# Optimization experiments

Hardware: AMD Instinct MI355X
Metric: run time of the kernel (lower is better)

The kernel has to match this reference:

```python
import jax, jax.numpy as jnp
import numpy as np

N_NODES = 100000
N_EDGES = 400000
IN_F, HID, OUT_F = 128, 1024, 64


def gcn_conv(x, src, dst, ew, W, b, n):
    # PyG GCNConv: add self-loops (weight 1), symmetric normalization,
    # out[dst] += norm * (x @ W)[src], then bias.
    loop = jnp.arange(n)
    s = jnp.concatenate([src, loop])
    d = jnp.concatenate([dst, loop])
    w = jnp.concatenate([ew, jnp.ones((n,), dtype=ew.dtype)])
    deg = jax.ops.segment_sum(w, d, num_segments=n)
    dinv = jnp.where(deg > 0, jax.lax.rsqrt(deg), 0.0)
    norm = dinv[s] * w * dinv[d]                      # [E+N]
    h = x @ W                                         # [N, out]
    out = jax.ops.segment_sum(h[s] * norm[:, None], d, num_segments=n)
    return out + b


def setup_inputs() -> dict:
    key = jax.random.key(0)
    k = jax.random.split(key, 8)
    x = jax.random.normal(k[0], (N_NODES, IN_F), dtype=jnp.float32)
    edge_index = jax.random.randint(k[1], (2, N_EDGES), 0, N_NODES, dtype=jnp.int64)
    edge_weight = jax.random.uniform(k[2], (N_EDGES,), dtype=jnp.float32)
    # Glorot-ish init for params
    W1 = jax.random.normal(k[3], (IN_F, HID), dtype=jnp.float32) * (1.0 / np.sqrt(IN_F))
    b1 = jnp.zeros((HID,), dtype=jnp.float32)
    W2 = jax.random.normal(k[4], (HID, OUT_F), dtype=jnp.float32) * (1.0 / np.sqrt(HID))
    b2 = jnp.zeros((OUT_F,), dtype=jnp.float32)
    return {"x": x, "edge_index": edge_index, "edge_weight": edge_weight,
            "W1": W1, "b1": b1, "W2": W2, "b2": b2}


def reference(x, edge_index, edge_weight, W1, b1, W2, b2):
    src, dst = edge_index[0], edge_index[1]
    h = gcn_conv(x, src, dst, edge_weight, W1, b1, N_NODES)
    h = jax.nn.relu(h)
    # F.dropout with training=False is identity (eval mode)
    out = gcn_conv(h, src, dst, edge_weight, W2, b2, N_NODES)
    return out
```

## Files before the change

### kernel.cpp

```cpp
#include <hip/hip_runtime.h>
#include <hip/hip_bf16.h>

#define N_NODES 100000
#define N_EDGES 400000
#define IN_F    128
#define HID     1024
#define OUT_F   64
#define BUCKET_CAP 24

typedef __attribute__((ext_vector_type(8))) short short8;
typedef __attribute__((ext_vector_type(4))) float floatx4;

__device__ inline unsigned short f2bf(float f) {
    unsigned int u = __float_as_uint(f);
    unsigned int r = u + 0x7FFF + ((u >> 16) & 1);
    return (unsigned short)(r >> 16);
}

__device__ inline unsigned int cvtpk(float a, float b) {
    union { __hip_bfloat162 h; unsigned int u; } v;
    v.h = __float22bfloat162_rn(float2{a, b});
    return v.u;
}

__device__ inline float bf2f(unsigned int lo16) {
    return __uint_as_float(lo16 << 16);
}

__device__ __forceinline__ void gload_lds16(const void* g, void* l) {
    __builtin_amdgcn_global_load_lds(
        (const __attribute__((address_space(1))) void*)g,
        (__attribute__((address_space(3))) void*)l, 16, 0, 0);
}

#define XB_BLOCKS  6250
#define WSB_BLOCKS 768
#define DEG_BLOCKS 1563

__global__ __launch_bounds__(256) void setup_kernel(
    const float* __restrict__ x, unsigned short* __restrict__ xb,
    const float* __restrict__ W1, const float* __restrict__ W2,
    unsigned short* __restrict__ S,
    const int* __restrict__ dst, const float* __restrict__ ew,
    float* __restrict__ deg)
{
    int b = blockIdx.x;
    int tid = threadIdx.x;
    if (b < XB_BLOCKS) {
        long i = (long)b * 256 + tid;
        float4 a = ((const float4*)x)[i * 2];
        float4 c = ((const float4*)x)[i * 2 + 1];
        ((uint4*)xb)[i] = make_uint4(cvtpk(a.x, a.y), cvtpk(a.z, a.w),
                                     cvtpk(c.x, c.y), cvtpk(c.z, c.w));
    } else if (b < XB_BLOCKS + WSB_BLOCKS) {
        int idx = b - XB_BLOCKS;
        int c = idx / 48;
        int r = (idx % 48) * 256 + tid;
        int f = r >> 9;
        int l = (r >> 3) & 63;
        int j = r & 7;
        float v;
        if (f < 16) {
            int nt = f >> 2, kt = f & 3;
            int hid = c * 64 + nt * 16 + (l & 15);
            int k   = kt * 32 + (l >> 4) * 8 + j;
            v = W1[(long)k * HID + hid];
        } else {
            int f2 = f - 16;
            int kb = f2 >> 2, nt2 = f2 & 3;
            int kh = c * 64 + kb * 32 + (j >> 2) * 16 + (l >> 4) * 4 + (j & 3);
            int oc = nt2 * 16 + (l & 15);
            v = W2[(long)kh * OUT_F + oc];
        }
        S[(long)c * 12288 + r] = f2bf(v);
    } else {
        int e = (b - XB_BLOCKS - WSB_BLOCKS) * 256 + tid;
        if (e < N_EDGES) atomicAdd(&deg[dst[e]], ew[e]);
    }
}

__global__ void fill_pairs_kernel(const int* __restrict__ src, const int* __restrict__ dst,
                                  const float* __restrict__ w, const float* __restrict__ deg,
                                  int* __restrict__ cnt, int2* __restrict__ pairs, int E) {
    int e = blockIdx.x * blockDim.x + threadIdx.x;
    if (e < E) {
        int s = src[e];
        int d = dst[e];
        float nv = rsqrtf(deg[s] + 1.0f) * w[e] * rsqrtf(deg[d] + 1.0f);
        int slot = atomicAdd(&cnt[d], 1);
        if (slot < BUCKET_CAP)
            pairs[(long)d * BUCKET_CAP + slot] = make_int2(s, __float_as_int(nv));
    }
}


__global__ __launch_bounds__(256) void gather128_kernel(
    const int2* __restrict__ pairs, const int* __restrict__ cnt,
    const float* __restrict__ deg, const unsigned short* __restrict__ xb,
    unsigned short* __restrict__ xab)
{
    int node = blockIdx.x * 16 + (threadIdx.x >> 4);
    int l = threadIdx.x & 15;
    float di = rsqrtf(deg[node] + 1.0f);
    float s = di * di;
    uint4 uv = ((const uint4*)(xb + (long)node * IN_F))[l];
    float acc[8];
    acc[0] = bf2f(uv.x & 0xffffu) * s; acc[1] = bf2f(uv.x >> 16) * s;
    acc[2] = bf2f(uv.y & 0xffffu) * s; acc[3] = bf2f(uv.y >> 16) * s;
    acc[4] = bf2f(uv.z & 0xffffu) * s; acc[5] = bf2f(uv.z >> 16) * s;
    acc[6] = bf2f(uv.w & 0xffffu) * s; acc[7] = bf2f(uv.w >> 16) * s;
    int c = cnt[node]; c = c < BUCKET_CAP ? c : BUCKET_CAP;
    const int2* p = pairs + (long)node * BUCKET_CAP;
    int j = 0;
    for (; j + 4 <= c; j += 4) {
        int4 q01 = *(const int4*)(p + j);
        int4 q23 = *(const int4*)(p + j + 2);
        uint4 u0 = ((const uint4*)(xb + (long)q01.x * IN_F))[l];
        uint4 u1 = ((const uint4*)(xb + (long)q01.z * IN_F))[l];
        uint4 u2 = ((const uint4*)(xb + (long)q23.x * IN_F))[l];
        uint4 u3 = ((const uint4*)(xb + (long)q23.z * IN_F))[l];
        float n0 = __int_as_float(q01.y), n1 = __int_as_float(q01.w);
        float n2 = __int_as_float(q23.y), n3 = __int_as_float(q23.w);
        acc[0] += n0 * bf2f(u0.x & 0xffffu) + n1 * bf2f(u1.x & 0xffffu)
                + n2 * bf2f(u2.x & 0xffffu) + n3 * bf2f(u3.x & 0xffffu);
        acc[1] += n0 * bf2f(u0.x >> 16) + n1 * bf2f(u1.x >> 16)
                + n2 * bf2f(u2.x >> 16) + n3 * bf2f(u3.x >> 16);
        acc[2] += n0 * bf2f(u0.y & 0xffffu) + n1 * bf2f(u1.y & 0xffffu)
                + n2 * bf2f(u2.y & 0xffffu) + n3 * bf2f(u3.y & 0xffffu);
        acc[3] += n0 * bf2f(u0.y >> 16) + n1 * bf2f(u1.y >> 16)
                + n2 * bf2f(u2.y >> 16) + n3 * bf2f(u3.y >> 16);
        acc[4] += n0 * bf2f(u0.z & 0xffffu) + n1 * bf2f(u1.z & 0xffffu)
                + n2 * bf2f(u2.z & 0xffffu) + n3 * bf2f(u3.z & 0xffffu);
        acc[5] += n0 * bf2f(u0.z >> 16) + n1 * bf2f(u1.z >> 16)
                + n2 * bf2f(u2.z >> 16) + n3 * bf2f(u3.z >> 16);
        acc[6] += n0 * bf2f(u0.w & 0xffffu) + n1 * bf2f(u1.w & 0xffffu)
                + n2 * bf2f(u2.w & 0xffffu) + n3 * bf2f(u3.w & 0xffffu);
        acc[7] += n0 * bf2f(u0.w >> 16) + n1 * bf2f(u1.w >> 16)
                + n2 * bf2f(u2.w >> 16) + n3 * bf2f(u3.w >> 16);
    }
    for (; j < c; j++) {
        int2 pp = p[j];
        float nv = __int_as_float(pp.y);
        uint4 u = ((const uint4*)(xb + (long)pp.x * IN_F))[l];
        acc[0] += nv * bf2f(u.x & 0xffffu); acc[1] += nv * bf2f(u.x >> 16);
        acc[2] += nv * bf2f(u.y & 0xffffu); acc[3] += nv * bf2f(u.y >> 16);
        acc[4] += nv * bf2f(u.z & 0xffffu); acc[5] += nv * bf2f(u.z >> 16);
        acc[6] += nv * bf2f(u.w & 0xffffu); acc[7] += nv * bf2f(u.w >> 16);
    }
    uint4 pk = make_uint4(cvtpk(acc[0], acc[1]), cvtpk(acc[2], acc[3]),
                          cvtpk(acc[4], acc[5]), cvtpk(acc[6], acc[7]));
    ((uint4*)(xab + (long)node * IN_F))[l] = pk;
}

__global__ __launch_bounds__(256) void gather64_kernel(
    const int2* __restrict__ pairs, const int* __restrict__ cnt,
    const float* __restrict__ deg, const unsigned short* __restrict__ tb,
    const float* __restrict__ bias, float* __restrict__ out)
{
    int node = blockIdx.x * 16 + (threadIdx.x >> 4);
    int l = threadIdx.x & 15;
    float di = rsqrtf(deg[node] + 1.0f);
    float s = di * di;
    uint2 tv = ((const uint2*)(tb + (long)node * OUT_F))[l];
    float4 bb = ((const float4*)bias)[l];
    float4 acc;
    acc.x = bf2f(tv.x & 0xffffu) * s + bb.x;
    acc.y = bf2f(tv.x >> 16) * s + bb.y;
    acc.z = bf2f(tv.y & 0xffffu) * s + bb.z;
    acc.w = bf2f(tv.y >> 16) * s + bb.w;
    int c = cnt[node]; c = c < BUCKET_CAP ? c : BUCKET_CAP;
    const int2* p = pairs + (long)node * BUCKET_CAP;
    int j = 0;
    for (; j + 4 <= c; j += 4) {
        int4 q01 = *(const int4*)(p + j);
        int4 q23 = *(const int4*)(p + j + 2);
        uint2 u0 = ((const uint2*)(tb + (long)q01.x * OUT_F))[l];
        uint2 u1 = ((const uint2*)(tb + (long)q01.z * OUT_F))[l];
        uint2 u2 = ((const uint2*)(tb + (long)q23.x * OUT_F))[l];
        uint2 u3 = ((const uint2*)(tb + (long)q23.z * OUT_F))[l];
        float n0 = __int_as_float(q01.y), n1 = __int_as_float(q01.w);
        float n2 = __int_as_float(q23.y), n3 = __int_as_float(q23.w);
        acc.x += n0 * bf2f(u0.x & 0xffffu) + n1 * bf2f(u1.x & 0xffffu)
               + n2 * bf2f(u2.x & 0xffffu) + n3 * bf2f(u3.x & 0xffffu);
        acc.y += n0 * bf2f(u0.x >> 16) + n1 * bf2f(u1.x >> 16)
               + n2 * bf2f(u2.x >> 16) + n3 * bf2f(u3.x >> 16);
        acc.z += n0 * bf2f(u0.y & 0xffffu) + n1 * bf2f(u1.y & 0xffffu)
               + n2 * bf2f(u2.y & 0xffffu) + n3 * bf2f(u3.y & 0xffffu);
        acc.w += n0 * bf2f(u0.y >> 16) + n1 * bf2f(u1.y >> 16)
               + n2 * bf2f(u2.y >> 16) + n3 * bf2f(u3.y >> 16);
    }
    for (; j < c; j++) {
        int2 pp = p[j];
        float nv = __int_as_float(pp.y);
        uint2 u = ((const uint2*)(tb + (long)pp.x * OUT_F))[l];
        acc.x += nv * bf2f(u.x & 0xffffu);
        acc.y += nv * bf2f(u.x >> 16);
        acc.z += nv * bf2f(u.y & 0xffffu);
        acc.w += nv * bf2f(u.y >> 16);
    }
    ((float4*)(out + (long)node * OUT_F))[l] = acc;
}


__global__ __launch_bounds__(512, 4) void fused_mlp_mfma_kernel(
    const unsigned short* __restrict__ Xb, const unsigned short* __restrict__ Wstream,
    const float* __restrict__ b1, unsigned short* __restrict__ Tb, int M)
{
    __shared__ unsigned short Wbuf[2][12288];

    const int tid = threadIdx.x;
    const int w   = tid >> 6;
    const int l   = tid & 63;
    const int lr  = l & 15;
    const int lq  = l >> 4;
    const long row0 = (long)blockIdx.x * 256 + w * 32;

    short8 bx[2][4];
    #pragma unroll
    for (int rt = 0; rt < 2; rt++) {
        long row = row0 + rt * 16 + lr;
        if (row < M) {
            const unsigned short* p = Xb + row * IN_F + lq * 8;
            #pragma unroll
            for (int kt = 0; kt < 4; kt++)
                bx[rt][kt] = *(const short8*)(p + kt * 32);
        } else {
            #pragma unroll
            for (int kt = 0; kt < 4; kt++)
                #pragma unroll
                for (int j = 0; j < 8; j++) bx[rt][kt][j] = 0;
        }
    }

    {
        const unsigned short* g = Wstream + (long)(w * 3) * 512 + l * 8;
        unsigned short* d = &Wbuf[0][(w * 3) * 512];
        #pragma unroll
        for (int s = 0; s < 3; s++)
            gload_lds16(g + s * 512, d + s * 512);
    }
    __syncthreads();

    floatx4 tacc[2][4];
    #pragma unroll
    for (int rt = 0; rt < 2; rt++)
        #pragma unroll
        for (int nt = 0; nt < 4; nt++)
            tacc[rt][nt] = (floatx4)0.0f;

    for (int c = 0; c < 16; c++) {
        const unsigned short* Wb = &Wbuf[c & 1][0];

        if (c < 15) {
            const unsigned short* g = Wstream + (long)(c + 1) * 12288 + (long)(w * 3) * 512 + l * 8;
            unsigned short* d = &Wbuf[(c + 1) & 1][(w * 3) * 512];
            #pragma unroll
            for (int s = 0; s < 3; s++)
                gload_lds16(g + s * 512, d + s * 512);
        }

        #pragma unroll
        for (int h = 0; h < 2; h++) {
            floatx4 hacc[2][2];
            #pragma unroll
            for (int rt = 0; rt < 2; rt++)
                #pragma unroll
                for (int n = 0; n < 2; n++)
                    hacc[rt][n] = (floatx4)0.0f;

            #pragma unroll
            for (int n = 0; n < 2; n++) {
                const int nt = h * 2 + n;
                short8 w1f[4];
                #pragma unroll
                for (int kt = 0; kt < 4; kt++)
                    w1f[kt] = *(const short8*)(Wb + (nt * 4 + kt) * 512 + l * 8);
                #pragma unroll
                for (int kt = 0; kt < 4; kt++) {
                    hacc[0][n] = __builtin_amdgcn_mfma_f32_16x16x32_bf16(w1f[kt], bx[0][kt], hacc[0][n], 0, 0, 0);
                    hacc[1][n] = __builtin_amdgcn_mfma_f32_16x16x32_bf16(w1f[kt], bx[1][kt], hacc[1][n], 0, 0, 0);
                }
            }

            floatx4 bb0 = *(const floatx4*)(b1 + c * 64 + (h * 2 + 0) * 16 + lq * 4);
            floatx4 bb1 = *(const floatx4*)(b1 + c * 64 + (h * 2 + 1) * 16 + lq * 4);
            short8 hf[2];
            #pragma unroll
            for (int rt = 0; rt < 2; rt++) {
                #pragma unroll
                for (int r = 0; r < 4; r++) {
                    hf[rt][r]     = (short)f2bf(fmaxf(hacc[rt][0][r] + bb0[r], 0.0f));
                    hf[rt][r + 4] = (short)f2bf(fmaxf(hacc[rt][1][r] + bb1[r], 0.0f));
                }
            }

            #pragma unroll
            for (int nt2 = 0; nt2 < 4; nt2++) {
                short8 w2f = *(const short8*)(Wb + (16 + h * 4 + nt2) * 512 + l * 8);
                tacc[0][nt2] = __builtin_amdgcn_mfma_f32_16x16x32_bf16(w2f, hf[0], tacc[0][nt2], 0, 0, 0);
                tacc[1][nt2] = __builtin_amdgcn_mfma_f32_16x16x32_bf16(w2f, hf[1], tacc[1][nt2], 0, 0, 0);
            }
        }

        if (c < 15) __syncthreads();
    }

    #pragma unroll
    for (int rt = 0; rt < 2; rt++) {
        long row = row0 + rt * 16 + lr;
        if (row < M) {
            #pragma unroll
            for (int nt = 0; nt < 4; nt++) {
                unsigned int q0 = (unsigned int)f2bf(tacc[rt][nt][0]) | ((unsigned int)f2bf(tacc[rt][nt][1]) << 16);
                unsigned int q1 = (unsigned int)f2bf(tacc[rt][nt][2]) | ((unsigned int)f2bf(tacc[rt][nt][3]) << 16);
                *(uint2*)(Tb + row * OUT_F + nt * 16 + lq * 4) = make_uint2(q0, q1);
            }
        }
    }
}


extern "C" void kernel_launch(void* const* d_in, const int* in_sizes, int n_in,
                              void* d_out, int out_size, void* d_ws, size_t ws_size,
                              hipStream_t stream) {
    const float* x   = (const float*)d_in[0];
    const int*   src = (const int*)d_in[1];
    const int*   dst = ((const int*)d_in[1]) + N_EDGES;
    const float* ew  = (const float*)d_in[2];
    const float* W1  = (const float*)d_in[3];
    const float* b1  = (const float*)d_in[4];
    const float* W2  = (const float*)d_in[5];
    const float* b2  = (const float*)d_in[6];
    float* out = (float*)d_out;

    float* ws     = (float*)d_ws;
    float* deg    = ws;
    int*   cnt    = (int*)(ws + 100096);
    int2*  pairs  = (int2*)(ws + 200192);
    unsigned short* xb  = (unsigned short*)(ws + 5000192);
    unsigned short* xab = (unsigned short*)(ws + 11400192);
    unsigned short* tb  = (unsigned short*)(ws + 17800192);
    unsigned short* wstream = (unsigned short*)(ws + 21000192);

    const int B = 256;

    hipMemsetAsync(ws, 0, 200192 * sizeof(float), stream);

    setup_kernel<<<XB_BLOCKS + WSB_BLOCKS + DEG_BLOCKS, B, 0, stream>>>(
        x, xb, W1, W2, wstream, dst, ew, deg);

    fill_pairs_kernel<<<(N_EDGES + B - 1) / B, B, 0, stream>>>(src, dst, ew, deg, cnt, pairs, N_EDGES);

    gather128_kernel<<<N_NODES / 16, 256, 0, stream>>>(pairs, cnt, deg, xb, xab);

    fused_mlp_mfma_kernel<<<(N_NODES + 255) / 256, 512, 0, stream>>>(
        xab, wstream, b1, tb, N_NODES);

    gather64_kernel<<<N_NODES / 16, 256, 0, stream>>>(pairs, cnt, deg, tb, b2, out);
}
```

Before: 156.7 us.

## Fuse first-layer neighbor aggregation into the MFMA MLP kernel

Removes the separate gather128 kernel. The fused MLP kernel now aggregates each row's normalized neighbor features straight into its bf16 A-fragment registers, which drops the intermediate xab buffer write and re-read and one kernel launch. The first W tile is issued to LDS before the gather so the two can overlap. In exchange, the gather runs with far fewer waves and a per-lane access pattern of 64-byte chunks with no edge unrolling, so it may become latency bound. Register pressure also rises, and launch bounds are relaxed from 4 to 2 blocks to allow for it.

Measured after the change: 152.4 us, median of 2. -2.7%, faster.

```diff
diff --git a/kernel.cpp b/kernel.cpp
--- a/kernel.cpp
+++ b/kernel.cpp
@@ -91,65 +91,6 @@
         if (slot < BUCKET_CAP)
             pairs[(long)d * BUCKET_CAP + slot] = make_int2(s, __float_as_int(nv));
     }
-}
-
-
-__global__ __launch_bounds__(256) void gather128_kernel(
-    const int2* __restrict__ pairs, const int* __restrict__ cnt,
-    const float* __restrict__ deg, const unsigned short* __restrict__ xb,
-    unsigned short* __restrict__ xab)
-{
-    int node = blockIdx.x * 16 + (threadIdx.x >> 4);
-    int l = threadIdx.x & 15;
-    float di = rsqrtf(deg[node] + 1.0f);
-    float s = di * di;
-    uint4 uv = ((const uint4*)(xb + (long)node * IN_F))[l];
-    float acc[8];
-    acc[0] = bf2f(uv.x & 0xffffu) * s; acc[1] = bf2f(uv.x >> 16) * s;
-    acc[2] = bf2f(uv.y & 0xffffu) * s; acc[3] = bf2f(uv.y >> 16) * s;
-    acc[4] = bf2f(uv.z & 0xffffu) * s; acc[5] = bf2f(uv.z >> 16) * s;
-    acc[6] = bf2f(uv.w & 0xffffu) * s; acc[7] = bf2f(uv.w >> 16) * s;
-    int c = cnt[node]; c = c < BUCKET_CAP ? c : BUCKET_CAP;
-    const int2* p = pairs + (long)node * BUCKET_CAP;
-    int j = 0;
-    for (; j + 4 <= c; j += 4) {
-        int4 q01 = *(const int4*)(p + j);
-        int4 q23 = *(const int4*)(p + j + 2);
-        uint4 u0 = ((const uint4*)(xb + (long)q01.x * IN_F))[l];
-        uint4 u1 = ((const uint4*)(xb + (long)q01.z * IN_F))[l];
-        uint4 u2 = ((const uint4*)(xb + (long)q23.x * IN_F))[l];
-        uint4 u3 = ((const uint4*)(xb + (long)q23.z * IN_F))[l];
-        float n0 = __int_as_float(q01.y), n1 = __int_as_float(q01.w);
-        float n2 = __int_as_float(q23.y), n3 = __int_as_float(q23.w);
-        acc[0] += n0 * bf2f(u0.x & 0xffffu) + n1 * bf2f(u1.x & 0xffffu)
-                + n2 * bf2f(u2.x & 0xffffu) + n3 * bf2f(u3.x & 0xffffu);
-        acc[1] += n0 * bf2f(u0.x >> 16) + n1 * bf2f(u1.x >> 16)
-                + n2 * bf2f(u2.x >> 16) + n3 * bf2f(u3.x >> 16);
-        acc[2] += n0 * bf2f(u0.y & 0xffffu) + n1 * bf2f(u1.y & 0xffffu)
-                + n2 * bf2f(u2.y & 0xffffu) + n3 * bf2f(u3.y & 0xffffu);
-        acc[3] += n0 * bf2f(u0.y >> 16) + n1 * bf2f(u1.y >> 16)
-                + n2 * bf2f(u2.y >> 16) + n3 * bf2f(u3.y >> 16);
-        acc[4] += n0 * bf2f(u0.z & 0xffffu) + n1 * bf2f(u1.z & 0xffffu)
-                + n2 * bf2f(u2.z & 0xffffu) + n3 * bf2f(u3.z & 0xffffu);
-        acc[5] += n0 * bf2f(u0.z >> 16) + n1 * bf2f(u1.z >> 16)
-                + n2 * bf2f(u2.z >> 16) + n3 * bf2f(u3.z >> 16);
-        acc[6] += n0 * bf2f(u0.w & 0xffffu) + n1 * bf2f(u1.w & 0xffffu)
-                + n2 * bf2f(u2.w & 0xffffu) + n3 * bf2f(u3.w & 0xffffu);
-        acc[7] += n0 * bf2f(u0.w >> 16) + n1 * bf2f(u1.w >> 16)
-                + n2 * bf2f(u2.w >> 16) + n3 * bf2f(u3.w >> 16);
-    }
-    for (; j < c; j++) {
-        int2 pp = p[j];
-        float nv = __int_as_float(pp.y);
-        uint4 u = ((const uint4*)(xb + (long)pp.x * IN_F))[l];
-        acc[0] += nv * bf2f(u.x & 0xffffu); acc[1] += nv * bf2f(u.x >> 16);
-        acc[2] += nv * bf2f(u.y & 0xffffu); acc[3] += nv * bf2f(u.y >> 16);
-        acc[4] += nv * bf2f(u.z & 0xffffu); acc[5] += nv * bf2f(u.z >> 16);
-        acc[6] += nv * bf2f(u.w & 0xffffu); acc[7] += nv * bf2f(u.w >> 16);
-    }
-    uint4 pk = make_uint4(cvtpk(acc[0], acc[1]), cvtpk(acc[2], acc[3]),
-                          cvtpk(acc[4], acc[5]), cvtpk(acc[6], acc[7]));
-    ((uint4*)(xab + (long)node * IN_F))[l] = pk;
 }
 
 __global__ __launch_bounds__(256) void gather64_kernel(
@@ -202,8 +143,10 @@
 }
 
 
-__global__ __launch_bounds__(512, 4) void fused_mlp_mfma_kernel(
-    const unsigned short* __restrict__ Xb, const unsigned short* __restrict__ Wstream,
+__global__ __launch_bounds__(512, 2) void fused_mlp_mfma_kernel(
+    const int2* __restrict__ pairs, const int* __restrict__ cnt,
+    const float* __restrict__ deg, const unsigned short* __restrict__ xb,
+    const unsigned short* __restrict__ Wstream,
     const float* __restrict__ b1, unsigned short* __restrict__ Tb, int M)
 {
     __shared__ unsigned short Wbuf[2][12288];
@@ -215,23 +158,6 @@
     const int lq  = l >> 4;
     const long row0 = (long)blockIdx.x * 256 + w * 32;
 
-    short8 bx[2][4];
-    #pragma unroll
-    for (int rt = 0; rt < 2; rt++) {
-        long row = row0 + rt * 16 + lr;
-        if (row < M) {
-            const unsigned short* p = Xb + row * IN_F + lq * 8;
-            #pragma unroll
-            for (int kt = 0; kt < 4; kt++)
-                bx[rt][kt] = *(const short8*)(p + kt * 32);
-        } else {
-            #pragma unroll
-            for (int kt = 0; kt < 4; kt++)
-                #pragma unroll
-                for (int j = 0; j < 8; j++) bx[rt][kt][j] = 0;
-        }
-    }
-
     {
         const unsigned short* g = Wstream + (long)(w * 3) * 512 + l * 8;
         unsigned short* d = &Wbuf[0][(w * 3) * 512];
@@ -239,6 +165,53 @@
         for (int s = 0; s < 3; s++)
             gload_lds16(g + s * 512, d + s * 512);
     }
+
+    short8 bx[2][4];
+    #pragma unroll
+    for (int rt = 0; rt < 2; rt++) {
+        long row = row0 + rt * 16 + lr;
+        if (row < M) {
+            float facc[4][8];
+            float di = rsqrtf(deg[row] + 1.0f);
+            float s = di * di;
+            const uint4* xrow = (const uint4*)(xb + row * IN_F);
+            #pragma unroll
+            for (int kt = 0; kt < 4; kt++) {
+                uint4 u = xrow[kt * 4 + lq];
+                facc[kt][0] = bf2f(u.x & 0xffffu) * s; facc[kt][1] = bf2f(u.x >> 16) * s;
+                facc[kt][2] = bf2f(u.y & 0xffffu) * s; facc[kt][3] = bf2f(u.y >> 16) * s;
+                facc[kt][4] = bf2f(u.z & 0xffffu) * s; facc[kt][5] = bf2f(u.z >> 16) * s;
+                facc[kt][6] = bf2f(u.w & 0xffffu) * s; facc[kt][7] = bf2f(u.w >> 16) * s;
+            }
+            int c = cnt[row]; c = c < BUCKET_CAP ? c : BUCKET_CAP;
+            const int2* p = pairs + (long)row * BUCKET_CAP;
+            for (int j = 0; j < c; j++) {
+                int2 pp = p[j];
+                float nv = __int_as_float(pp.y);
+                const uint4* srow = (const uint4*)(xb + (long)pp.x * IN_F);
+                #pragma unroll
+                for (int kt = 0; kt < 4; kt++) {
+                    uint4 u = srow[kt * 4 + lq];
+                    facc[kt][0] += nv * bf2f(u.x & 0xffffu); facc[kt][1] += nv * bf2f(u.x >> 16);
+                    facc[kt][2] += nv * bf2f(u.y & 0xffffu); facc[kt][3] += nv * bf2f(u.y >> 16);
+                    facc[kt][4] += nv * bf2f(u.z & 0xffffu); facc[kt][5] += nv * bf2f(u.z >> 16);
+                    facc[kt][6] += nv * bf2f(u.w & 0xffffu); facc[kt][7] += nv * bf2f(u.w >> 16);
+                }
+            }
+            #pragma unroll
+            for (int kt = 0; kt < 4; kt++)
+                #pragma unroll
+                for (int i = 0; i < 8; i++)
+                    bx[rt][kt][i] = (short)f2bf(facc[kt][i]);
+        } else {
+            #pragma unroll
+            for (int kt = 0; kt < 4; kt++)
+                #pragma unroll
+                for (int i = 0; i < 8; i++)
+                    bx[rt][kt][i] = 0;
+        }
+    }
+
     __syncthreads();
 
     floatx4 tacc[2][4];
@@ -338,9 +311,8 @@
     int*   cnt    = (int*)(ws + 100096);
     int2*  pairs  = (int2*)(ws + 200192);
     unsigned short* xb  = (unsigned short*)(ws + 5000192);
-    unsigned short* xab = (unsigned short*)(ws + 11400192);
-    unsigned short* tb  = (unsigned short*)(ws + 17800192);
-    unsigned short* wstream = (unsigned short*)(ws + 21000192);
+    unsigned short* tb  = (unsigned short*)(ws + 11400192);
+    unsigned short* wstream = (unsigned short*)(ws + 14600192);
 
     const int B = 256;
 
@@ -351,10 +323,8 @@
 
     fill_pairs_kernel<<<(N_EDGES + B - 1) / B, B, 0, stream>>>(src, dst, ew, deg, cnt, pairs, N_EDGES);
 
-    gather128_kernel<<<N_NODES / 16, 256, 0, stream>>>(pairs, cnt, deg, xb, xab);
-
     fused_mlp_mfma_kernel<<<(N_NODES + 255) / 256, 512, 0, stream>>>(
-        xab, wstream, b1, tb, N_NODES);
+        pairs, cnt, deg, xb, wstream, b1, tb, N_NODES);
 
     gather64_kernel<<<N_NODES / 16, 256, 0, stream>>>(pairs, cnt, deg, tb, b2, out);
 }
```
